# Kernel tuning notes

Hardware: AMD Instinct MI355X
Metric: run time of the kernel (lower is better)

Reference implementation:

```python
import jax, jax.numpy as jnp
import numpy as np

B, H, S, HD = 4, 8, 2048, 64   # batch, heads, seq, head_dim (num_out_feats//num_heads)
D_IN = 512                      # num_in_feats (projector output width)
D_CAT = H * HD                  # projector input width


def setup_inputs() -> dict:
    key = jax.random.key(0)
    kq, kk, kv, kw, kb = jax.random.split(key, 5)
    q = jax.random.normal(kq, (B, H, S, HD), dtype=jnp.float32)
    k = jax.random.normal(kk, (B, H, S, HD), dtype=jnp.float32)
    v = jax.random.normal(kv, (B, H, S, HD), dtype=jnp.float32)
    # torch Linear(D_CAT, D_IN): weight [D_IN, D_CAT], bias [D_IN]
    W = jax.random.normal(kw, (D_IN, D_CAT), dtype=jnp.float32) * 0.02
    bias = jax.random.normal(kb, (D_IN,), dtype=jnp.float32) * 0.02
    return {"q": q, "k": k, "v": v, "W": W, "bias": bias}


def reference(q, k, v, W, bias):
    head_dim = q.shape[-1]
    scale = jnp.asarray(1.0 / np.sqrt(head_dim), dtype=q.dtype)
    # scores: [b, h, sq, sk], single stable softmax
    scores = jax.nn.softmax(jnp.einsum('bhqd,bhkd->bhqk', q, k) * scale, axis=-1)
    # AV: the original broadcast-multiply-sum is mathematically a matmul
    o = jnp.einsum('bhqk,bhkd->bhqd', scores, v)  # [b, h, s, hd]
    b, h, s, d = o.shape
    # faithful to torch .view(b, s, -1) on a contiguous [b,h,s,d] buffer: raw reshape (no head transpose)
    o = o.reshape(b, s, h * d)
    return o @ W.T + bias
```

## Files before the change

kernel.cpp:

```cpp
#include <hip/hip_runtime.h>

#define BATCH 4
#define NH    8
#define SEQ   2048
#define HDIM  64
#define DIN   512
#define DCAT  512
#define NBH   (BATCH*NH)
#define NT    32

typedef __attribute__((ext_vector_type(8))) short short8;
typedef __attribute__((ext_vector_type(4))) float f32x4;
typedef __attribute__((ext_vector_type(16))) float f32x16;
typedef __attribute__((ext_vector_type(4))) unsigned int uint4v;
typedef __attribute__((ext_vector_type(2))) unsigned int uint2v;
typedef unsigned short u16;
typedef unsigned int u32;

#define ZERO16 (f32x16){0.f,0.f,0.f,0.f,0.f,0.f,0.f,0.f,0.f,0.f,0.f,0.f,0.f,0.f,0.f,0.f}

__device__ inline u32 cvtpk(float lo, float hi) {
    u32 r;
    asm("v_cvt_pk_bf16_f32 %0, %1, %2" : "=v"(r) : "v"(lo), "v"(hi));
    return r;
}

__device__ inline void glds16(const void* g, void* l) {
    __builtin_amdgcn_global_load_lds(
        (const __attribute__((address_space(1))) u32*)g,
        (__attribute__((address_space(3))) u32*)l, 16, 0, 0);
}

__global__ __launch_bounds__(256)
void vt_prepass(const float* __restrict__ vg, u16* __restrict__ vt) {
    const int bh = blockIdx.x, tb = blockIdx.y, t = threadIdx.x;
    __shared__ float Ls[32][65];
    const float* vp = vg + ((size_t)bh * SEQ + tb * 32) * HDIM;
    {
        int r = t >> 3, c8 = (t & 7) * 8;
        float4 f0 = *reinterpret_cast<const float4*>(vp + r * HDIM + c8);
        float4 f1 = *reinterpret_cast<const float4*>(vp + r * HDIM + c8 + 4);
        Ls[r][c8+0] = f0.x; Ls[r][c8+1] = f0.y; Ls[r][c8+2] = f0.z; Ls[r][c8+3] = f0.w;
        Ls[r][c8+4] = f1.x; Ls[r][c8+5] = f1.y; Ls[r][c8+6] = f1.z; Ls[r][c8+7] = f1.w;
    }
    __syncthreads();
    u16* wt = vt + ((size_t)bh * 64 + tb) * 2048;
    {
        int r = t >> 3, p = t & 7;
        int sL = p ^ (r & 7);
        int d  = (sL >> 2) * 32 + r;
        int j0 = (sL & 3) * 8;
        uint4v u;
        u.x = cvtpk(Ls[j0+0][d], Ls[j0+1][d]);
        u.y = cvtpk(Ls[j0+2][d], Ls[j0+3][d]);
        u.z = cvtpk(Ls[j0+4][d], Ls[j0+5][d]);
        u.w = cvtpk(Ls[j0+6][d], Ls[j0+7][d]);
        *reinterpret_cast<uint4v*>(wt + r * 64 + p * 8) = u;
    }
}

__global__ __launch_bounds__(512, 4)
void attn_mfma(const float* __restrict__ qg, const float* __restrict__ kg,
               const u16* __restrict__ vtg, u16* __restrict__ og) {
    const int bh  = blockIdx.x;
    const int qB  = blockIdx.y * 128;
    const int tid = threadIdx.x;
    const int w = tid >> 6, lane = tid & 63;
    const int qc = w & 3, half = w >> 2;
    const int r  = lane & 31;
    const int hi = lane >> 5;
    const bool hib = hi != 0;

    __shared__ char sh[33792];
    auto Kb = [&](int h, int b) { return sh + (h*2 + b) * 4096; };
    auto Vb = [&](int h, int b) { return sh + 16384 + (h*2 + b) * 4096; };

    const size_t base = (size_t)bh * SEQ * HDIM;

    const float qs = 0.125f * 1.44269504088896f;
    short8 qb[4];
#pragma unroll
    for (int ks = 0; ks < 4; ++ks) {
        const float* qp = qg + base + (size_t)(qB + qc*32 + r) * HDIM + ks*16 + hi*8;
        float4 f0 = *reinterpret_cast<const float4*>(qp);
        float4 f1 = *reinterpret_cast<const float4*>(qp + 4);
        uint4v u;
        u.x = cvtpk(f0.x * qs, f0.y * qs);
        u.y = cvtpk(f0.z * qs, f0.w * qs);
        u.z = cvtpk(f1.x * qs, f1.y * qs);
        u.w = cvtpk(f1.z * qs, f1.w * qs);
        qb[ks] = __builtin_bit_cast(short8, u);
    }

    const int srow = tid >> 4;
    const int sp4  = tid & 15;
    const int kwoff = srow*128 + ((((sp4 >> 1) ^ (srow & 7)) << 4) | ((sp4 & 1) << 3));
    const float* kgp0 = kg + base + (size_t)srow * HDIM + sp4 * 4;
    const float* kgp1 = kgp0 + (size_t)1024 * HDIM;
    const int vh  = tid >> 8;
    const int vls = (tid & 255) * 16;
    const u16* vsrc = vtg + (size_t)bh * 64 * 2048 + (size_t)(vh * 32) * 2048 + (tid & 255) * 8;

    f32x16 ot[2] = { ZERO16, ZERO16 };
    float l = 0.f;

    float4 kr0, kr1;
    kr0 = *reinterpret_cast<const float4*>(kgp0);
    kr1 = *reinterpret_cast<const float4*>(kgp1);
    glds16(vsrc, Vb(vh, 0) + vls);
    {
        uint2v u0, u1;
        u0.x = cvtpk(kr0.x, kr0.y); u0.y = cvtpk(kr0.z, kr0.w);
        u1.x = cvtpk(kr1.x, kr1.y); u1.y = cvtpk(kr1.z, kr1.w);
        *reinterpret_cast<uint2v*>(Kb(0,0) + kwoff) = u0;
        *reinterpret_cast<uint2v*>(Kb(1,0) + kwoff) = u1;
    }
    kr0 = *reinterpret_cast<const float4*>(kgp0 + 2048);
    kr1 = *reinterpret_cast<const float4*>(kgp1 + 2048);
    asm volatile("s_waitcnt vmcnt(2) lgkmcnt(0)" ::: "memory");
    __builtin_amdgcn_s_barrier();
    glds16(vsrc + 2048, Vb(vh, 1) + vls);

    for (int t = 0; t < NT; ++t) {
        const int b = t & 1;
        const char* Kc = Kb(half, b);
        const char* Vc = Vb(half, b);

        f32x16 st = ZERO16;
        __builtin_amdgcn_s_setprio(1);
#pragma unroll
        for (int ks = 0; ks < 4; ++ks) {
            short8 ka = *reinterpret_cast<const short8*>(
                Kc + r*128 + (((ks*2 + hi) ^ (r & 7)) << 4));
            st = __builtin_amdgcn_mfma_f32_32x32x16_bf16(ka, qb[ks], st, 0, 0, 0);
        }
        __builtin_amdgcn_s_setprio(0);

        u32 pw[8];
        float lp = 0.f;
#pragma unroll
        for (int j = 0; j < 8; ++j) {
            float p0 = __builtin_amdgcn_exp2f(st[2*j]);
            float p1 = __builtin_amdgcn_exp2f(st[2*j+1]);
            lp += p0 + p1;
            pw[j] = cvtpk(p0, p1);
        }
        l += lp;

        u32 xw[8];
#pragma unroll
        for (int j = 0; j < 8; ++j) xw[j] = (u32)__shfl_xor((int)pw[j], 32);

        uint4v b0, b1;
        b0.x = hib ? xw[2] : pw[0];  b0.y = hib ? xw[3] : pw[1];
        b0.z = hib ? pw[2] : xw[0];  b0.w = hib ? pw[3] : xw[1];
        b1.x = hib ? xw[6] : pw[4];  b1.y = hib ? xw[7] : pw[5];
        b1.z = hib ? pw[6] : xw[4];  b1.w = hib ? pw[7] : xw[5];
        short8 pb[2] = { __builtin_bit_cast(short8, b0), __builtin_bit_cast(short8, b1) };

        __builtin_amdgcn_s_setprio(1);
#pragma unroll
        for (int dt = 0; dt < 2; ++dt)
#pragma unroll
        for (int ks = 0; ks < 2; ++ks) {
            short8 va = *reinterpret_cast<const short8*>(
                Vc + r*128 + (((dt*4 + ks*2 + hi) ^ (r & 7)) << 4));
            ot[dt] = __builtin_amdgcn_mfma_f32_32x32x16_bf16(va, pb[ks], ot[dt], 0, 0, 0);
        }
        __builtin_amdgcn_s_setprio(0);

        if (t + 1 < NT) {
            uint2v u0, u1;
            u0.x = cvtpk(kr0.x, kr0.y); u0.y = cvtpk(kr0.z, kr0.w);
            u1.x = cvtpk(kr1.x, kr1.y); u1.y = cvtpk(kr1.z, kr1.w);
            *reinterpret_cast<uint2v*>(Kb(0, b ^ 1) + kwoff) = u0;
            *reinterpret_cast<uint2v*>(Kb(1, b ^ 1) + kwoff) = u1;
        }
        if (t + 2 < NT) {
            kr0 = *reinterpret_cast<const float4*>(kgp0 + (size_t)(t + 2) * 2048);
            kr1 = *reinterpret_cast<const float4*>(kgp1 + (size_t)(t + 2) * 2048);
        }
        if (t < NT - 2)
            asm volatile("s_waitcnt vmcnt(2) lgkmcnt(0)" ::: "memory");
        else
            asm volatile("s_waitcnt vmcnt(0) lgkmcnt(0)" ::: "memory");
        __builtin_amdgcn_s_barrier();
        if (t + 2 < NT)
            glds16(vsrc + (size_t)(t + 2) * 2048, Vb(vh, b) + vls);
    }

    l += __shfl_xor(l, 32);

    float* dumpF = (float*)(sh + (w & 3) * 8192) + lane * 32;
    float* dumpL = (float*)(sh + 32768) + (w & 3) * 64;
    if (w >= 4) {
#pragma unroll
        for (int dt = 0; dt < 2; ++dt)
#pragma unroll
        for (int jj = 0; jj < 4; ++jj) {
            f32x4 c = { ot[dt][jj*4+0], ot[dt][jj*4+1], ot[dt][jj*4+2], ot[dt][jj*4+3] };
            *reinterpret_cast<f32x4*>(dumpF + dt*16 + jj*4) = c;
        }
        dumpL[lane] = l;
    }
    __syncthreads();
    if (w < 4) {
#pragma unroll
        for (int dt = 0; dt < 2; ++dt)
#pragma unroll
        for (int jj = 0; jj < 4; ++jj) {
            f32x4 c = *reinterpret_cast<const f32x4*>(dumpF + dt*16 + jj*4);
            ot[dt][jj*4+0] += c[0]; ot[dt][jj*4+1] += c[1];
            ot[dt][jj*4+2] += c[2]; ot[dt][jj*4+3] += c[3];
        }
        float ltot = l + dumpL[lane];
        float inv  = 1.0f / ltot;
        asm volatile("s_waitcnt lgkmcnt(0)" ::: "memory");
        __builtin_amdgcn_sched_barrier(0);
        u16* ta = (u16*)(sh + w * 8192);
#pragma unroll
        for (int dt = 0; dt < 2; ++dt)
#pragma unroll
        for (int j = 0; j < 8; ++j) {
            u32 wd = cvtpk(ot[dt][2*j] * inv, ot[dt][2*j+1] * inv);
            int d = dt*32 + ((2*j) & 3) + 8*((2*j) >> 2) + 4*hi;
            *reinterpret_cast<u32*>((char*)ta + r*144 + d*2) = wd;
        }
        asm volatile("s_waitcnt lgkmcnt(0)" ::: "memory");
        __builtin_amdgcn_sched_barrier(0);
#pragma unroll
        for (int s = 0; s < 4; ++s) {
            int idx = lane + s*64;
            int rr = idx >> 3, j = idx & 7;
            uint4v u = *reinterpret_cast<const uint4v*>((char*)ta + rr*144 + j*16);
            *reinterpret_cast<uint4v*>(
                og + ((size_t)bh * SEQ + qB + w*32 + rr) * HDIM + j*8) = u;
        }
    }
}

__global__ __launch_bounds__(256)
void proj_mfma(const u16* __restrict__ X, const float* __restrict__ Wg,
               const float* __restrict__ bias, float* __restrict__ out) {
    const int g0 = blockIdx.x * 128;
    const int n0 = blockIdx.y * 64;
    const int tid = threadIdx.x;
    const int w = tid >> 6, lane = tid & 63;
    const int c = lane & 15, gq = lane >> 4;
    const int cx = c & 7;

    __shared__ char sh[49152];
    u16* const XbA = (u16*)(sh);
    u16* const XbB = (u16*)(sh + 16384);
    u16* const WbA = (u16*)(sh + 32768);
    u16* const WbB = (u16*)(sh + 40960);

    const int wn0 = tid >> 3, wp = tid & 7;

    f32x4 acc[2][4];
#pragma unroll
    for (int mt = 0; mt < 2; ++mt)
#pragma unroll
    for (int nt = 0; nt < 4; ++nt) acc[mt][nt] = (f32x4){0.f,0.f,0.f,0.f};

    float4 w0a, w0b, w1a, w1b;

    auto loadW = [&](int kt) {
        const float* p0 = Wg + (size_t)(n0 + wn0) * DCAT + kt*64 + ((wp ^ (wn0 & 7)) * 8);
        const float* p1 = Wg + (size_t)(n0 + 32 + wn0) * DCAT + kt*64 + ((wp ^ ((32 + wn0) & 7)) * 8);
        w0a = *reinterpret_cast<const float4*>(p0);
        w0b = *reinterpret_cast<const float4*>(p0 + 4);
        w1a = *reinterpret_cast<const float4*>(p1);
        w1b = *reinterpret_cast<const float4*>(p1 + 4);
    };
    auto writeW = [&](u16* Wb) {
        uint4v u;
        u.x = cvtpk(w0a.x, w0a.y); u.y = cvtpk(w0a.z, w0a.w);
        u.z = cvtpk(w0b.x, w0b.y); u.w = cvtpk(w0b.z, w0b.w);
        *reinterpret_cast<uint4v*>((char*)Wb + wn0*128 + wp*16) = u;
        u.x = cvtpk(w1a.x, w1a.y); u.y = cvtpk(w1a.z, w1a.w);
        u.z = cvtpk(w1b.x, w1b.y); u.w = cvtpk(w1b.z, w1b.w);
        *reinterpret_cast<uint4v*>((char*)Wb + (32 + wn0)*128 + wp*16) = u;
    };
    auto issueX = [&](int kt, u16* Xb) {
#pragma unroll
        for (int i = 0; i < 4; ++i) {
            int s = w*256 + i*64 + lane;
            int rr = s >> 3, p = s & 7;
            glds16(X + (size_t)(g0 + rr) * DCAT + kt*64 + ((p ^ (rr & 7)) * 8),
                   (char*)Xb + w*4096 + i*1024);
        }
    };

    loadW(0);
    issueX(0, XbA);
    writeW(WbA);
    loadW(1);
    issueX(1, XbB);
    asm volatile("s_waitcnt vmcnt(8) lgkmcnt(0)" ::: "memory");
    __builtin_amdgcn_s_barrier();

    for (int kt = 0; kt < 8; ++kt) {
        u16* const Xc = (kt & 1) ? XbB : XbA;
        u16* const Wc = (kt & 1) ? WbB : WbA;
        u16* const Wn = (kt & 1) ? WbA : WbB;

        __builtin_amdgcn_s_setprio(1);
#pragma unroll
        for (int ks = 0; ks < 2; ++ks) {
            short8 a0 = *reinterpret_cast<const short8*>(
                (char*)Xc + (w*32 + c)*128 + (((ks*4 + gq) ^ cx) << 4));
            short8 a1 = *reinterpret_cast<const short8*>(
                (char*)Xc + (w*32 + 16 + c)*128 + (((ks*4 + gq) ^ cx) << 4));
#pragma unroll
            for (int nt = 0; nt < 4; ++nt) {
                short8 bb = *reinterpret_cast<const short8*>(
                    (char*)Wc + (nt*16 + c)*128 + (((ks*4 + gq) ^ cx) << 4));
                acc[0][nt] = __builtin_amdgcn_mfma_f32_16x16x32_bf16(a0, bb, acc[0][nt], 0,0,0);
                acc[1][nt] = __builtin_amdgcn_mfma_f32_16x16x32_bf16(a1, bb, acc[1][nt], 0,0,0);
            }
        }
        __builtin_amdgcn_s_setprio(0);

        if (kt + 1 < 8) writeW(Wn);
        if (kt + 2 < 8) loadW(kt + 2);
        if (kt < 6)
            asm volatile("s_waitcnt vmcnt(4) lgkmcnt(0)" ::: "memory");
        else
            asm volatile("s_waitcnt vmcnt(0) lgkmcnt(0)" ::: "memory");
        __builtin_amdgcn_s_barrier();
        if (kt + 2 < 8) issueX(kt + 2, Xc);
    }

    float bv[4];
#pragma unroll
    for (int nt = 0; nt < 4; ++nt) bv[nt] = bias[n0 + nt*16 + c];
#pragma unroll
    for (int mt = 0; mt < 2; ++mt)
#pragma unroll
    for (int nt = 0; nt < 4; ++nt)
#pragma unroll
    for (int rr = 0; rr < 4; ++rr)
        out[(size_t)(g0 + w*32 + mt*16 + gq*4 + rr) * DIN + n0 + nt*16 + c] =
            acc[mt][nt][rr] + bv[nt];
}

extern "C" void kernel_launch(void* const* d_in, const int* in_sizes, int n_in,
                              void* d_out, int out_size, void* d_ws, size_t ws_size,
                              hipStream_t stream) {
    (void)in_sizes; (void)n_in; (void)out_size; (void)ws_size;
    const float* q    = (const float*)d_in[0];
    const float* k    = (const float*)d_in[1];
    const float* v    = (const float*)d_in[2];
    const float* W    = (const float*)d_in[3];
    const float* bias = (const float*)d_in[4];

    u16* vt = (u16*)d_ws;
    u16* ob = vt + (size_t)NBH * 64 * 2048;

    vt_prepass<<<dim3(NBH, 64), 256, 0, stream>>>(v, vt);
    attn_mfma <<<dim3(NBH, SEQ/128), 512, 0, stream>>>(q, k, vt, ob);
    proj_mfma <<<dim3((BATCH*SEQ)/128, DIN/64), 256, 0, stream>>>(ob, W, bias, (float*)d_out);
}
```

Before: 77.13 us.

## Pre-convert K to bf16 in prepass, widen per-wave Q tile, use permlane swap

```diff
diff --git a/kernel.cpp b/kernel.cpp
--- a/kernel.cpp
+++ b/kernel.cpp
@@ -13,7 +13,6 @@
 typedef __attribute__((ext_vector_type(4))) float f32x4;
 typedef __attribute__((ext_vector_type(16))) float f32x16;
 typedef __attribute__((ext_vector_type(4))) unsigned int uint4v;
-typedef __attribute__((ext_vector_type(2))) unsigned int uint2v;
 typedef unsigned short u16;
 typedef unsigned int u32;
 
@@ -25,6 +24,10 @@
     return r;
 }
 
+__device__ inline void plswap(u32 &a, u32 &b) {
+    asm volatile("v_permlane32_swap_b32 %0, %1" : "+v"(a), "+v"(b));
+}
+
 __device__ inline void glds16(const void* g, void* l) {
     __builtin_amdgcn_global_load_lds(
         (const __attribute__((address_space(1))) u32*)g,
@@ -32,56 +35,67 @@
 }
 
 __global__ __launch_bounds__(256)
-void vt_prepass(const float* __restrict__ vg, u16* __restrict__ vt) {
-    const int bh = blockIdx.x, tb = blockIdx.y, t = threadIdx.x;
+void kv_prepass(const float* __restrict__ kg, const float* __restrict__ vg,
+                u16* __restrict__ kws, u16* __restrict__ vws) {
+    const int tb = blockIdx.x;
+    const int bh = blockIdx.y;
+    const int t  = threadIdx.x;
+    const size_t gbase = ((size_t)bh * SEQ + tb * 32) * HDIM;
+
+    {
+        int srow = t >> 3, j = t & 7;
+        const float* kp = kg + gbase + srow * HDIM + j * 8;
+        float4 f0 = *reinterpret_cast<const float4*>(kp);
+        float4 f1 = *reinterpret_cast<const float4*>(kp + 4);
+        uint4v u;
+        u.x = cvtpk(f0.x, f0.y); u.y = cvtpk(f0.z, f0.w);
+        u.z = cvtpk(f1.x, f1.y); u.w = cvtpk(f1.z, f1.w);
+        *reinterpret_cast<uint4v*>(kws + ((size_t)bh*64 + tb)*2048 + srow*64 + (j ^ (srow & 7))*8) = u;
+    }
+
     __shared__ float Ls[32][65];
-    const float* vp = vg + ((size_t)bh * SEQ + tb * 32) * HDIM;
     {
-        int r = t >> 3, c8 = (t & 7) * 8;
-        float4 f0 = *reinterpret_cast<const float4*>(vp + r * HDIM + c8);
-        float4 f1 = *reinterpret_cast<const float4*>(vp + r * HDIM + c8 + 4);
-        Ls[r][c8+0] = f0.x; Ls[r][c8+1] = f0.y; Ls[r][c8+2] = f0.z; Ls[r][c8+3] = f0.w;
-        Ls[r][c8+4] = f1.x; Ls[r][c8+5] = f1.y; Ls[r][c8+6] = f1.z; Ls[r][c8+7] = f1.w;
+        int rr = t >> 3, c8 = (t & 7) * 8;
+        float4 f0 = *reinterpret_cast<const float4*>(vg + gbase + rr * HDIM + c8);
+        float4 f1 = *reinterpret_cast<const float4*>(vg + gbase + rr * HDIM + c8 + 4);
+        Ls[rr][c8+0] = f0.x; Ls[rr][c8+1] = f0.y; Ls[rr][c8+2] = f0.z; Ls[rr][c8+3] = f0.w;
+        Ls[rr][c8+4] = f1.x; Ls[rr][c8+5] = f1.y; Ls[rr][c8+6] = f1.z; Ls[rr][c8+7] = f1.w;
     }
     __syncthreads();
-    u16* wt = vt + ((size_t)bh * 64 + tb) * 2048;
     {
-        int r = t >> 3, p = t & 7;
-        int sL = p ^ (r & 7);
-        int d  = (sL >> 2) * 32 + r;
+        int rr = t >> 3, p = t & 7;
+        int sL = p ^ (rr & 7);
+        int d  = (sL >> 2) * 32 + rr;
         int j0 = (sL & 3) * 8;
         uint4v u;
         u.x = cvtpk(Ls[j0+0][d], Ls[j0+1][d]);
         u.y = cvtpk(Ls[j0+2][d], Ls[j0+3][d]);
         u.z = cvtpk(Ls[j0+4][d], Ls[j0+5][d]);
         u.w = cvtpk(Ls[j0+6][d], Ls[j0+7][d]);
-        *reinterpret_cast<uint4v*>(wt + r * 64 + p * 8) = u;
-    }
-}
-
-__global__ __launch_bounds__(512, 4)
-void attn_mfma(const float* __restrict__ qg, const float* __restrict__ kg,
-               const u16* __restrict__ vtg, u16* __restrict__ og) {
-    const int bh  = blockIdx.x;
-    const int qB  = blockIdx.y * 128;
+        *reinterpret_cast<uint4v*>(vws + ((size_t)bh*64 + tb)*2048 + rr*64 + p*8) = u;
+    }
+}
+
+__global__ __launch_bounds__(256, 2)
+void attn_mfma(const float* __restrict__ qg, const u16* __restrict__ kws,
+               const u16* __restrict__ vws, u16* __restrict__ og) {
+    const int qB  = blockIdx.x * 128;
+    const int bh  = blockIdx.y;
     const int tid = threadIdx.x;
     const int w = tid >> 6, lane = tid & 63;
-    const int qc = w & 3, half = w >> 2;
+    const int qw = w & 1, hf = w >> 1;
     const int r  = lane & 31;
     const int hi = lane >> 5;
-    const bool hib = hi != 0;
 
     __shared__ char sh[33792];
-    auto Kb = [&](int h, int b) { return sh + (h*2 + b) * 4096; };
-    auto Vb = [&](int h, int b) { return sh + 16384 + (h*2 + b) * 4096; };
-
-    const size_t base = (size_t)bh * SEQ * HDIM;
 
     const float qs = 0.125f * 1.44269504088896f;
-    short8 qb[4];
+    short8 qb[2][4];
+#pragma unroll
+    for (int sub = 0; sub < 2; ++sub)
 #pragma unroll
     for (int ks = 0; ks < 4; ++ks) {
-        const float* qp = qg + base + (size_t)(qB + qc*32 + r) * HDIM + ks*16 + hi*8;
+        const float* qp = qg + ((size_t)bh * SEQ + qB + qw*64 + sub*32 + r) * HDIM + ks*16 + hi*8;
         float4 f0 = *reinterpret_cast<const float4*>(qp);
         float4 f1 = *reinterpret_cast<const float4*>(qp + 4);
         uint4v u;
@@ -89,152 +103,153 @@
         u.y = cvtpk(f0.z * qs, f0.w * qs);
         u.z = cvtpk(f1.x * qs, f1.y * qs);
         u.w = cvtpk(f1.z * qs, f1.w * qs);
-        qb[ks] = __builtin_bit_cast(short8, u);
-    }
-
-    const int srow = tid >> 4;
-    const int sp4  = tid & 15;
-    const int kwoff = srow*128 + ((((sp4 >> 1) ^ (srow & 7)) << 4) | ((sp4 & 1) << 3));
-    const float* kgp0 = kg + base + (size_t)srow * HDIM + sp4 * 4;
-    const float* kgp1 = kgp0 + (size_t)1024 * HDIM;
-    const int vh  = tid >> 8;
-    const int vls = (tid & 255) * 16;
-    const u16* vsrc = vtg + (size_t)bh * 64 * 2048 + (size_t)(vh * 32) * 2048 + (tid & 255) * 8;
-
-    f32x16 ot[2] = { ZERO16, ZERO16 };
-    float l = 0.f;
-
-    float4 kr0, kr1;
-    kr0 = *reinterpret_cast<const float4*>(kgp0);
-    kr1 = *reinterpret_cast<const float4*>(kgp1);
-    glds16(vsrc, Vb(vh, 0) + vls);
-    {
-        uint2v u0, u1;
-        u0.x = cvtpk(kr0.x, kr0.y); u0.y = cvtpk(kr0.z, kr0.w);
-        u1.x = cvtpk(kr1.x, kr1.y); u1.y = cvtpk(kr1.z, kr1.w);
-        *reinterpret_cast<uint2v*>(Kb(0,0) + kwoff) = u0;
-        *reinterpret_cast<uint2v*>(Kb(1,0) + kwoff) = u1;
-    }
-    kr0 = *reinterpret_cast<const float4*>(kgp0 + 2048);
-    kr1 = *reinterpret_cast<const float4*>(kgp1 + 2048);
-    asm volatile("s_waitcnt vmcnt(2) lgkmcnt(0)" ::: "memory");
+        qb[sub][ks] = __builtin_bit_cast(short8, u);
+    }
+
+    const short8 ones8 = __builtin_bit_cast(short8,
+        (uint4v){0x3f803f80u, 0x3f803f80u, 0x3f803f80u, 0x3f803f80u});
+
+    const u16* kbase = kws + (size_t)bh * 64 * 2048 + (size_t)tid * 8;
+    const u16* vbase = vws + (size_t)bh * 64 * 2048 + (size_t)tid * 8;
+    auto stage = [&](int t, int db) {
+        glds16(kbase + (size_t)t * 2048,        sh + db*4096 + tid*16);
+        glds16(kbase + (size_t)(32 + t) * 2048, sh + (2 + db)*4096 + tid*16);
+        glds16(vbase + (size_t)t * 2048,        sh + 16384 + db*4096 + tid*16);
+        glds16(vbase + (size_t)(32 + t) * 2048, sh + 16384 + (2 + db)*4096 + tid*16);
+    };
+
+    f32x16 otA0 = ZERO16, otA1 = ZERO16, otB0 = ZERO16, otB1 = ZERO16;
+    f32x16 lcA = ZERO16, lcB = ZERO16;
+
+    asm volatile("s_waitcnt vmcnt(0)" ::: "memory");
+    stage(0, 0);
+    stage(1, 1);
+    asm volatile("s_waitcnt vmcnt(4) lgkmcnt(0)" ::: "memory");
     __builtin_amdgcn_s_barrier();
-    glds16(vsrc + 2048, Vb(vh, 1) + vls);
 
     for (int t = 0; t < NT; ++t) {
-        const int b = t & 1;
-        const char* Kc = Kb(half, b);
-        const char* Vc = Vb(half, b);
-
-        f32x16 st = ZERO16;
+        const int db = t & 1;
+        const char* Kc = sh + (hf*2 + db)*4096;
+        const char* Vc = sh + 16384 + (hf*2 + db)*4096;
+
+        f32x16 stA = ZERO16, stB = ZERO16;
         __builtin_amdgcn_s_setprio(1);
 #pragma unroll
         for (int ks = 0; ks < 4; ++ks) {
             short8 ka = *reinterpret_cast<const short8*>(
                 Kc + r*128 + (((ks*2 + hi) ^ (r & 7)) << 4));
-            st = __builtin_amdgcn_mfma_f32_32x32x16_bf16(ka, qb[ks], st, 0, 0, 0);
+            stA = __builtin_amdgcn_mfma_f32_32x32x16_bf16(ka, qb[0][ks], stA, 0, 0, 0);
+            stB = __builtin_amdgcn_mfma_f32_32x32x16_bf16(ka, qb[1][ks], stB, 0, 0, 0);
         }
         __builtin_amdgcn_s_setprio(0);
 
-        u32 pw[8];
-        float lp = 0.f;
+        u32 pwA[8], pwB[8];
 #pragma unroll
         for (int j = 0; j < 8; ++j) {
-            float p0 = __builtin_amdgcn_exp2f(st[2*j]);
-            float p1 = __builtin_amdgcn_exp2f(st[2*j+1]);
-            lp += p0 + p1;
-            pw[j] = cvtpk(p0, p1);
-        }
-        l += lp;
-
-        u32 xw[8];
-#pragma unroll
-        for (int j = 0; j < 8; ++j) xw[j] = (u32)__shfl_xor((int)pw[j], 32);
-
-        uint4v b0, b1;
-        b0.x = hib ? xw[2] : pw[0];  b0.y = hib ? xw[3] : pw[1];
-        b0.z = hib ? pw[2] : xw[0];  b0.w = hib ? pw[3] : xw[1];
-        b1.x = hib ? xw[6] : pw[4];  b1.y = hib ? xw[7] : pw[5];
-        b1.z = hib ? pw[6] : xw[4];  b1.w = hib ? pw[7] : xw[5];
-        short8 pb[2] = { __builtin_bit_cast(short8, b0), __builtin_bit_cast(short8, b1) };
+            pwA[j] = cvtpk(__builtin_amdgcn_exp2f(stA[2*j]), __builtin_amdgcn_exp2f(stA[2*j+1]));
+            pwB[j] = cvtpk(__builtin_amdgcn_exp2f(stB[2*j]), __builtin_amdgcn_exp2f(stB[2*j+1]));
+        }
+        plswap(pwA[0], pwA[2]); plswap(pwA[1], pwA[3]);
+        plswap(pwA[4], pwA[6]); plswap(pwA[5], pwA[7]);
+        plswap(pwB[0], pwB[2]); plswap(pwB[1], pwB[3]);
+        plswap(pwB[4], pwB[6]); plswap(pwB[5], pwB[7]);
+        short8 pbA0 = __builtin_bit_cast(short8, (uint4v){pwA[0], pwA[1], pwA[2], pwA[3]});
+        short8 pbA1 = __builtin_bit_cast(short8, (uint4v){pwA[4], pwA[5], pwA[6], pwA[7]});
+        short8 pbB0 = __builtin_bit_cast(short8, (uint4v){pwB[0], pwB[1], pwB[2], pwB[3]});
+        short8 pbB1 = __builtin_bit_cast(short8, (uint4v){pwB[4], pwB[5], pwB[6], pwB[7]});
 
         __builtin_amdgcn_s_setprio(1);
-#pragma unroll
-        for (int dt = 0; dt < 2; ++dt)
-#pragma unroll
-        for (int ks = 0; ks < 2; ++ks) {
-            short8 va = *reinterpret_cast<const short8*>(
-                Vc + r*128 + (((dt*4 + ks*2 + hi) ^ (r & 7)) << 4));
-            ot[dt] = __builtin_amdgcn_mfma_f32_32x32x16_bf16(va, pb[ks], ot[dt], 0, 0, 0);
+        lcA = __builtin_amdgcn_mfma_f32_32x32x16_bf16(ones8, pbA0, lcA, 0, 0, 0);
+        lcB = __builtin_amdgcn_mfma_f32_32x32x16_bf16(ones8, pbB0, lcB, 0, 0, 0);
+        {
+            short8 va = *reinterpret_cast<const short8*>(Vc + r*128 + (((0*4 + 0*2 + hi) ^ (r & 7)) << 4));
+            otA0 = __builtin_amdgcn_mfma_f32_32x32x16_bf16(va, pbA0, otA0, 0, 0, 0);
+            otB0 = __builtin_amdgcn_mfma_f32_32x32x16_bf16(va, pbB0, otB0, 0, 0, 0);
+        }
+        {
+            short8 va = *reinterpret_cast<const short8*>(Vc + r*128 + (((1*4 + 0*2 + hi) ^ (r & 7)) << 4));
+            otA1 = __builtin_amdgcn_mfma_f32_32x32x16_bf16(va, pbA0, otA1, 0, 0, 0);
+            otB1 = __builtin_amdgcn_mfma_f32_32x32x16_bf16(va, pbB0, otB1, 0, 0, 0);
+        }
+        lcA = __builtin_amdgcn_mfma_f32_32x32x16_bf16(ones8, pbA1, lcA, 0, 0, 0);
+        lcB = __builtin_amdgcn_mfma_f32_32x32x16_bf16(ones8, pbB1, lcB, 0, 0, 0);
+        {
+            short8 va = *reinterpret_cast<const short8*>(Vc + r*128 + (((0*4 + 1*2 + hi) ^ (r & 7)) << 4));
+            otA0 = __builtin_amdgcn_mfma_f32_32x32x16_bf16(va, pbA1, otA0, 0, 0, 0);
+            otB0 = __builtin_amdgcn_mfma_f32_32x32x16_bf16(va, pbB1, otB0, 0, 0, 0);
+        }
+        {
+            short8 va = *reinterpret_cast<const short8*>(Vc + r*128 + (((1*4 + 1*2 + hi) ^ (r & 7)) << 4));
+            otA1 = __builtin_amdgcn_mfma_f32_32x32x16_bf16(va, pbA1, otA1, 0, 0, 0);
+            otB1 = __builtin_amdgcn_mfma_f32_32x32x16_bf16(va, pbB1, otB1, 0, 0, 0);
         }
         __builtin_amdgcn_s_setprio(0);
 
-        if (t + 1 < NT) {
-            uint2v u0, u1;
-            u0.x = cvtpk(kr0.x, kr0.y); u0.y = cvtpk(kr0.z, kr0.w);
-            u1.x = cvtpk(kr1.x, kr1.y); u1.y = cvtpk(kr1.z, kr1.w);
-            *reinterpret_cast<uint2v*>(Kb(0, b ^ 1) + kwoff) = u0;
-            *reinterpret_cast<uint2v*>(Kb(1, b ^ 1) + kwoff) = u1;
-        }
-        if (t + 2 < NT) {
-            kr0 = *reinterpret_cast<const float4*>(kgp0 + (size_t)(t + 2) * 2048);
-            kr1 = *reinterpret_cast<const float4*>(kgp1 + (size_t)(t + 2) * 2048);
-        }
-        if (t < NT - 2)
-            asm volatile("s_waitcnt vmcnt(2) lgkmcnt(0)" ::: "memory");
-        else
-            asm volatile("s_waitcnt vmcnt(0) lgkmcnt(0)" ::: "memory");
+        asm volatile("s_waitcnt vmcnt(0) lgkmcnt(0)" ::: "memory");
         __builtin_amdgcn_s_barrier();
-        if (t + 2 < NT)
-            glds16(vsrc + (size_t)(t + 2) * 2048, Vb(vh, b) + vls);
-    }
-
-    l += __shfl_xor(l, 32);
-
-    float* dumpF = (float*)(sh + (w & 3) * 8192) + lane * 32;
-    float* dumpL = (float*)(sh + 32768) + (w & 3) * 64;
-    if (w >= 4) {
-#pragma unroll
-        for (int dt = 0; dt < 2; ++dt)
+        if (t + 2 < NT) stage(t + 2, db);
+    }
+
+    __syncthreads();
+    char* dump = sh + qw * 16384;
+    float* larea = (float*)(sh + 32768) + qw * 64;
+
+    if (hf == 1) {
 #pragma unroll
         for (int jj = 0; jj < 4; ++jj) {
-            f32x4 c = { ot[dt][jj*4+0], ot[dt][jj*4+1], ot[dt][jj*4+2], ot[dt][jj*4+3] };
-            *reinterpret_cast<f32x4*>(dumpF + dt*16 + jj*4) = c;
-        }
-        dumpL[lane] = l;
+            *reinterpret_cast<f32x4*>(dump + (0*4 + jj)*1024 + lane*16) =
+                (f32x4){otA0[jj*4+0], otA0[jj*4+1], otA0[jj*4+2], otA0[jj*4+3]};
+            *reinterpret_cast<f32x4*>(dump + (1*4 + jj)*1024 + lane*16) =
+                (f32x4){otA1[jj*4+0], otA1[jj*4+1], otA1[jj*4+2], otA1[jj*4+3]};
+            *reinterpret_cast<f32x4*>(dump + (2*4 + jj)*1024 + lane*16) =
+                (f32x4){otB0[jj*4+0], otB0[jj*4+1], otB0[jj*4+2], otB0[jj*4+3]};
+            *reinterpret_cast<f32x4*>(dump + (3*4 + jj)*1024 + lane*16) =
+                (f32x4){otB1[jj*4+0], otB1[jj*4+1], otB1[jj*4+2], otB1[jj*4+3]};
+        }
+        larea[r]      = lcA[0];
+        larea[32 + r] = lcB[0];
     }
     __syncthreads();
-    if (w < 4) {
-#pragma unroll
-        for (int dt = 0; dt < 2; ++dt)
+    if (hf == 0) {
 #pragma unroll
         for (int jj = 0; jj < 4; ++jj) {
-            f32x4 c = *reinterpret_cast<const f32x4*>(dumpF + dt*16 + jj*4);
-            ot[dt][jj*4+0] += c[0]; ot[dt][jj*4+1] += c[1];
-            ot[dt][jj*4+2] += c[2]; ot[dt][jj*4+3] += c[3];
-        }
-        float ltot = l + dumpL[lane];
-        float inv  = 1.0f / ltot;
+            f32x4 c0 = *reinterpret_cast<const f32x4*>(dump + (0*4 + jj)*1024 + lane*16);
+            f32x4 c1 = *reinterpret_cast<const f32x4*>(dump + (1*4 + jj)*1024 + lane*16);
+            f32x4 c2 = *reinterpret_cast<const f32x4*>(dump + (2*4 + jj)*1024 + lane*16);
+            f32x4 c3 = *reinterpret_cast<const f32x4*>(dump + (3*4 + jj)*1024 + lane*16);
+#pragma unroll
+            for (int e = 0; e < 4; ++e) {
+                otA0[jj*4+e] += c0[e]; otA1[jj*4+e] += c1[e];
+                otB0[jj*4+e] += c2[e]; otB1[jj*4+e] += c3[e];
+            }
+        }
+        float invA = 1.0f / (lcA[0] + larea[r]);
+        float invB = 1.0f / (lcB[0] + larea[32 + r]);
+
         asm volatile("s_waitcnt lgkmcnt(0)" ::: "memory");
         __builtin_amdgcn_sched_barrier(0);
-        u16* ta = (u16*)(sh + w * 8192);
-#pragma unroll
-        for (int dt = 0; dt < 2; ++dt)
+        char* ta = dump;
 #pragma unroll
         for (int j = 0; j < 8; ++j) {
-            u32 wd = cvtpk(ot[dt][2*j] * inv, ot[dt][2*j+1] * inv);
-            int d = dt*32 + ((2*j) & 3) + 8*((2*j) >> 2) + 4*hi;
-            *reinterpret_cast<u32*>((char*)ta + r*144 + d*2) = wd;
+            int dbase = ((2*j) & 3) + 8*((2*j) >> 2) + 4*hi;
+            u32 wA0 = cvtpk(otA0[2*j] * invA, otA0[2*j+1] * invA);
+            u32 wA1 = cvtpk(otA1[2*j] * invA, otA1[2*j+1] * invA);
+            u32 wB0 = cvtpk(otB0[2*j] * invB, otB0[2*j+1] * invB);
+            u32 wB1 = cvtpk(otB1[2*j] * invB, otB1[2*j+1] * invB);
+            *reinterpret_cast<u32*>(ta + (0*32 + r)*144 + (0*32 + dbase)*2) = wA0;
+            *reinterpret_cast<u32*>(ta + (0*32 + r)*144 + (1*32 + dbase)*2) = wA1;
+            *reinterpret_cast<u32*>(ta + (1*32 + r)*144 + (0*32 + dbase)*2) = wB0;
+            *reinterpret_cast<u32*>(ta + (1*32 + r)*144 + (1*32 + dbase)*2) = wB1;
         }
         asm volatile("s_waitcnt lgkmcnt(0)" ::: "memory");
         __builtin_amdgcn_sched_barrier(0);
 #pragma unroll
-        for (int s = 0; s < 4; ++s) {
-            int idx = lane + s*64;
+        for (int i = 0; i < 8; ++i) {
+            int idx = i * 64 + lane;
             int rr = idx >> 3, j = idx & 7;
-            uint4v u = *reinterpret_cast<const uint4v*>((char*)ta + rr*144 + j*16);
+            uint4v u = *reinterpret_cast<const uint4v*>(ta + rr*144 + j*16);
             *reinterpret_cast<uint4v*>(
-                og + ((size_t)bh * SEQ + qB + w*32 + rr) * HDIM + j*8) = u;
+                og + ((size_t)bh * SEQ + qB + qw*64 + rr) * HDIM + j*8) = u;
         }
     }
 }
@@ -355,10 +370,11 @@
     const float* W    = (const float*)d_in[3];
     const float* bias = (const float*)d_in[4];
 
-    u16* vt = (u16*)d_ws;
-    u16* ob = vt + (size_t)NBH * 64 * 2048;
-
-    vt_prepass<<<dim3(NBH, 64), 256, 0, stream>>>(v, vt);
-    attn_mfma <<<dim3(NBH, SEQ/128), 512, 0, stream>>>(q, k, vt, ob);
+    u16* kws = (u16*)d_out;
+    u16* vws = (u16*)d_ws;
+    u16* ob  = vws + (size_t)NBH * 64 * 2048;
+
+    kv_prepass<<<dim3(64, NBH), 256, 0, stream>>>(k, v, kws, vws);
+    attn_mfma <<<dim3(16, NBH), 256, 0, stream>>>(q, kws, vws, ob);
     proj_mfma <<<dim3((BATCH*SEQ)/128, DIN/64), 256, 0, stream>>>(ob, W, bias, (float*)d_out);
 }
```

After: 69.53 us. -9.9%, faster.
